# Kernel tuning notes

Measured on AMD Instinct MI355X. Metric: run time of the kernel, lower is better.

Reference implementation:

```python
import jax, jax.numpy as jnp
import numpy as np

B, M, F_IN, DX, K, L, N_ALL = 8192, 10, 128, 128, 64, 32, 100000
NN = M - 1          # n_neigh
INF = float(M)


def layer_norm(x, g, b, eps=1e-5):
    mu = x.mean(-1, keepdims=True)
    var = ((x - mu) ** 2).mean(-1, keepdims=True)
    return (x - mu) * jax.lax.rsqrt(var + eps) * g + b


def bfs_dists(adj, mask):
    # normalized all-pairs hop distances via repeated boolean matmul (m=10 fixed)
    adj_bin = (adj > 1e-5).astype(jnp.float32)
    eye = jnp.eye(M, dtype=bool)
    d = jnp.where(eye[None], 0.0, jnp.where(adj_bin > 0, 1.0, INF))
    curr = adj_bin
    for k in range(2, M):
        curr = jnp.matmul(curr, adj_bin)
        d = jnp.where((curr > 0) & (d == INF), float(k), d)
    mask2 = mask[:, :, None] * mask[:, None, :]
    d = jnp.where(mask2 == 0, INF, d)
    return d / float(M)


def compute_sw(zb, zp, theta, vmask):
    # sliced Wasserstein-2 between batch point clouds [B,NN,d] and prototypes [K,NN,d]
    tn = theta / jnp.linalg.norm(theta, axis=1, keepdims=True)
    pb = jnp.einsum('bmd,ld->bml', zb, tn)
    pp = jnp.einsum('kmd,ld->kml', zp, tn)
    idx = jnp.argsort(pb, axis=1)
    pbs = jnp.take_along_axis(pb, idx, axis=1)
    pps = jnp.sort(pp, axis=1)
    w = jnp.take_along_axis(jnp.broadcast_to(vmask[:, :, None], pb.shape), idx, axis=1)
    w = w / (w.sum(axis=1, keepdims=True) + 1e-9)
    # sum_m w*(pb-pp)^2 expanded to avoid materializing [B,K,NN,L]
    t1 = (w * pbs ** 2).sum(axis=1)                   # [B,L]
    t2 = jnp.einsum('bml,kml->bkl', w * pbs, pps)     # [B,K,L]
    t3 = jnp.einsum('bml,kml->bkl', w, pps ** 2)
    return (t1[:, None, :] - 2.0 * t2 + t3).mean(axis=-1)


def compute_radial(rb, rp, vmask):
    idx = jnp.argsort(rb, axis=1)
    rbs = jnp.take_along_axis(rb, idx, axis=1)
    rps = jnp.sort(rp, axis=1)
    w = jnp.take_along_axis(vmask, idx, axis=1)
    w = w / (w.sum(axis=1, keepdims=True) + 1e-9)
    return (((rbs[:, None, :] - rps[None]) ** 2) * w[:, None, :]).sum(-1)


def setup_inputs() -> dict:
    key = jax.random.key(0)
    ks = jax.random.split(key, 16)
    up = (jax.random.uniform(ks[0], (B, M, M)) < 0.3).astype(jnp.float32)
    adj = jnp.maximum(up, up.transpose(0, 2, 1)) * (1.0 - jnp.eye(M))
    features = jax.random.normal(ks[1], (N_ALL, F_IN), jnp.float32)
    idxs = jax.random.randint(ks[2], (B, M), 0, N_ALL + 1)   # N_ALL == padding index
    rn = lambda k, s, sc=0.02: sc * jax.random.normal(k, s, jnp.float32)
    params = dict(
        x_lin_w=rn(ks[3], (F_IN, DX), 0.05), x_lin_b=jnp.zeros((DX,)),
        x_ln_g=jnp.ones((DX,)), x_ln_b=jnp.zeros((DX,)),
        s_ln_g=jnp.ones((NN,)), s_ln_b=jnp.zeros((NN,)),
        theta_x=jax.random.normal(ks[4], (L, DX), jnp.float32),
        theta_s=jax.random.normal(ks[5], (L, NN), jnp.float32),
        alpha_raw=jnp.zeros(()),
        an_w1=rn(ks[6], (DX, 32), 0.1), an_b1=jnp.zeros((32,)),
        an_w2=rn(ks[7], (32, 1), 0.1), an_b2=jnp.zeros((1,)),
        wn_w1=rn(ks[8], (2 * DX, 32), 0.1), wn_b1=jnp.zeros((32,)),
        wn_w2=rn(ks[9], (32, 1), 0.1), wn_b2=jnp.zeros((1,)),
        w_raw=jnp.zeros(()),
        proto_root=jax.random.normal(ks[10], (K, F_IN), jnp.float32),
        proto_neigh=jax.random.normal(ks[11], (K, NN, F_IN), jnp.float32),
        proto_rad=jax.random.uniform(ks[12], (K, NN)),
        proto_dn=jax.random.uniform(ks[13], (NN * (NN - 1) // 2, K), minval=-0.5, maxval=0.5),
        log_gamma=jnp.asarray(np.log(0.01), jnp.float32),
    )
    return {"adj": adj, "features": features, "idxs": idxs, **params}


def reference(adj, features, idxs, x_lin_w, x_lin_b, x_ln_g, x_ln_b, s_ln_g, s_ln_b,
              theta_x, theta_s, alpha_raw, an_w1, an_b1, an_w2, an_b2,
              wn_w1, wn_b1, wn_w2, wn_b2, w_raw,
              proto_root, proto_neigh, proto_rad, proto_dn, log_gamma):
    b = adj.shape[0]
    x_all = jnp.concatenate([features, jnp.zeros((1, F_IN), features.dtype)], 0)
    x_patch = x_all[idxs]                             # [B,M,F]
    x_root, x_neigh = x_patch[:, 0], x_patch[:, 1:]
    vmask = (idxs[:, 1:] != N_ALL).astype(jnp.float32)   # [B,NN]
    lin = lambda x: x @ x_lin_w + x_lin_b
    h_root = layer_norm(lin(x_root), x_ln_g, x_ln_b)
    h_proto_root = layer_norm(lin(proto_root), x_ln_g, x_ln_b)
    d_root_feat = (jnp.sum(h_root ** 2, -1)[:, None] + jnp.sum(h_proto_root ** 2, -1)[None]
                   - 2.0 * h_root @ h_proto_root.T)   # squared cdist [B,K]
    full_mask = jnp.concatenate([jnp.ones((b, 1), jnp.float32), vmask], 1)
    dists_full = bfs_dists(adj, full_mask)
    d_radial_str = compute_radial(dists_full[:, 0, 1:], proto_rad, vmask)
    h_neigh = layer_norm(lin(x_neigh), x_ln_g, x_ln_b)     # dropout = identity (eval)
    h_proto_neigh = layer_norm(lin(proto_neigh), x_ln_g, x_ln_b)
    sw_neigh_feat = compute_sw(h_neigh, h_proto_neigh, theta_x, vmask)
    hs_neigh = layer_norm(jnp.sort(dists_full[:, 1:, 1:], axis=1), s_ln_g, s_ln_b)
    ti, tj = np.triu_indices(NN, 1)
    C = jnp.zeros((K, NN, NN)).at[:, ti, tj].set(jax.nn.sigmoid(proto_dn).T)
    C = C + C.transpose(0, 2, 1)
    hs_proto = layer_norm(jnp.sort(C, axis=1), s_ln_g, s_ln_b)
    sw_neigh_str = compute_sw(hs_neigh, hs_proto, theta_s, vmask)
    h_pooled = (h_neigh * vmask[:, :, None]).sum(1) / (vmask.sum(1, keepdims=True) + 1e-9)
    alpha_logit = jnp.maximum(h_pooled @ an_w1 + an_b1, 0.0) @ an_w2 + an_b2   # [B,1]
    alpha = jax.nn.sigmoid(alpha_raw + alpha_logit)
    # pairwise w_net([h_root; h_proto_root]) without materializing [B,K,2*DX]
    hb = h_root @ wn_w1[:DX] + wn_b1                   # [B,32]
    hp = h_proto_root @ wn_w1[DX:]                     # [K,32]
    w_logit = (jnp.maximum(hb[:, None] + hp[None], 0.0) @ wn_w2)[..., 0] + wn_b2[0]
    w = jax.nn.sigmoid(w_raw + w_logit)                # [B,K]
    d_feat = w * d_root_feat + (1.0 - w) * sw_neigh_feat
    d_str = w * d_radial_str + (1.0 - w) * sw_neigh_str
    d_fgw = alpha * d_feat + (1.0 - alpha) * d_str
    return jnp.exp(-jnp.exp(log_gamma) * d_fgw)        # [B,K]
```

## Files before the change

### kernel.cpp

```cpp
#include <hip/hip_runtime.h>
#include <hip/hip_bf16.h>

typedef unsigned short u16;
typedef __attribute__((ext_vector_type(8))) short short8;
typedef __attribute__((ext_vector_type(4))) float f32x4;

#define NN 9
#define DX 128
#define KP 64
#define LL 32
#define NALL 100000
#define BMAX 8192
#define NBM 16
#define NBP 64

#define MFMA(a, b, c) __builtin_amdgcn_mfma_f32_16x16x32_bf16(a, b, c, 0, 0, 0)
#define WFENCE() __threadfence_block()

__device__ __align__(16) float g_tns[LL * NN];
__device__ __align__(16) float g_hprn[KP];
__device__ __align__(16) float g_hpt[32 * KP];
__device__ __align__(16) float g_rpst[NN * KP];
__device__ __align__(16) u16   g_hx[BMAX * 10 * DX];
__device__ __align__(16) u16   g_pW[16384];
__device__ __align__(16) u16   g_pBt[4096];
__device__ __align__(16) u16   g_pBr[8192];
__device__ __align__(16) u16   g_pBx[36864];
__device__ __align__(16) u16   g_pBs[36864];
__device__ __align__(16) u16   g_pAn[4096];
__device__ __align__(16) u16   g_pWn[4096];

__device__ __forceinline__ float bf2f(u16 u) {
    union { unsigned u; float f; } v; v.u = ((unsigned)u) << 16; return v.f;
}
__device__ __forceinline__ u16 f2bf(float f) {
    __hip_bfloat16 h = __float2bfloat16(f);
    union { __hip_bfloat16 h; u16 u; } v; v.h = h; return v.u;
}
__device__ __forceinline__ float ldv(const void* p, long i, int f32) {
    return f32 ? ((const float*)p)[i] : bf2f(((const u16*)p)[i]);
}
__device__ __forceinline__ float sigmoidf(float x) { return 1.f / (1.f + expf(-x)); }

__device__ __forceinline__ int bfrag_idx(int ksteps, int ncol, int kd) {
    int ntile = ncol >> 4, n = ncol & 15;
    int kstep = kd >> 5, quad = (kd >> 3) & 3, j = kd & 7;
    return ((ntile * ksteps + kstep) * 64 + quad * 16 + n) * 8 + j;
}

__device__ __forceinline__ void rank9(const float* v, int* r) {
#pragma unroll
    for (int m = 0; m < 9; m++) {
        int rk = 0;
#pragma unroll
        for (int n = 0; n < 9; n++)
            rk += (v[n] < v[m]) || (v[n] == v[m] && n < m);
        r[m] = rk;
    }
}

__global__ __launch_bounds__(256) void k_pack(
    const void* xlw, const void* theta_x, const void* theta_s,
    const void* an_w1, const void* wn_w1, const void* xlg) {
    int t = threadIdx.x;
    const int f32 = (((const u16*)xlg)[0] == 0);
    if (blockIdx.x == 0) {
        for (int i = t; i < 16384; i += 256) {
            int c = i >> 7, d = i & 127;
            g_pW[bfrag_idx(4, d, c)] = f2bf(ldv(xlw, i, f32));
        }
    } else if (blockIdx.x == 1) {
        if (t < 32) {
            float s = 0;
            for (int d = 0; d < 128; d++) { float v = ldv(theta_x, t * 128 + d, f32); s = fmaf(v, v, s); }
            float inv = 1.f / sqrtf(s);
            for (int d = 0; d < 128; d++)
                g_pBt[bfrag_idx(4, t, d)] = f2bf(ldv(theta_x, t * 128 + d, f32) * inv);
        } else if (t < 64) {
            int l = t - 32;
            float s = 0;
            for (int j = 0; j < 9; j++) { float v = ldv(theta_s, l * 9 + j, f32); s = fmaf(v, v, s); }
            float inv = 1.f / sqrtf(s);
            for (int j = 0; j < 9; j++) g_tns[l * 9 + j] = ldv(theta_s, l * 9 + j, f32) * inv;
        }
    } else {
        for (int i = t; i < 4096; i += 256) {
            int d = i >> 5, j = i & 31;
            g_pAn[bfrag_idx(4, j, d)] = f2bf(ldv(an_w1, i, f32));
            g_pWn[bfrag_idx(4, j, d)] = f2bf(ldv(wn_w1, i, f32));
        }
    }
}

__global__ __launch_bounds__(256, 8) void k_lin(
    const void* feat, const int* idxs,
    const void* proto_root, const void* proto_neigh,
    const void* xlb, const void* xlg, const void* xlbt,
    const void* slg, const void* slb, const void* wn_w1,
    const void* proto_rad, const void* proto_dn, int B) {
    __shared__ __align__(16) unsigned char sm[4368];
    u16*   hXpb = (u16*)sm;
    float* pbX  = (float*)(sm + 2560);
    float* Cm   = (float*)(sm + 3712);
    float* hsnP = (float*)(sm + 4040);

    int t = threadIdx.x, lane = t & 63, w = t >> 6;
    const int f32 = (((const u16*)xlg)[0] == 0);
    int fm = lane & 15, quad = lane >> 4;
    bool isProto = (blockIdx.x < (unsigned)NBP);
    int rcap = isProto ? 10 : 60;
    int base = isProto ? blockIdx.x * 10 : (blockIdx.x - NBP) * 60;
    int rowT = isProto ? KP * 10 : B * 10;

    int lr = w * 16 + fm, gr = base + lr;
    bool azero = true;
    const void* abuf = feat; long aoff = 0;
    if (lr < rcap && gr < rowT) {
        if (!isProto) {
            int id = idxs[gr];
            if (id != NALL) { azero = false; aoff = (long)id * 128; }
        } else {
            int rr = gr % 10; azero = false;
            if (rr < 9) { abuf = proto_neigh; aoff = (long)((gr / 10) * 9 + rr) * 128; }
            else        { abuf = proto_root;  aoff = (long)(gr / 10) * 128; }
        }
    }

    if (w * 16 < rcap) {
        f32x4 acc[8];
#pragma unroll
        for (int nt = 0; nt < 8; nt++) acc[nt] = (f32x4){0.f, 0.f, 0.f, 0.f};
#pragma unroll
        for (int ks = 0; ks < 4; ks++) {
            short8 af = {0, 0, 0, 0, 0, 0, 0, 0};
            if (!azero) {
                if (f32) {
                    const f32x4* src = (const f32x4*)((const float*)abuf + aoff + ks * 32 + quad * 8);
                    f32x4 v0 = src[0], v1 = src[1];
                    u16* ap = (u16*)&af;
#pragma unroll
                    for (int j = 0; j < 4; j++) { ap[j] = f2bf(v0[j]); ap[4 + j] = f2bf(v1[j]); }
                } else {
                    af = *(const short8*)((const u16*)abuf + aoff + ks * 32 + quad * 8);
                }
            }
#pragma unroll
            for (int nt = 0; nt < 8; nt++) {
                short8 bf = *(const short8*)(g_pW + ((nt * 4 + ks) * 64 + lane) * 8);
                acc[nt] = MFMA(af, bf, acc[nt]);
            }
        }
        float bias8[8];
#pragma unroll
        for (int nt = 0; nt < 8; nt++) bias8[nt] = ldv(xlb, nt * 16 + fm, f32);
#pragma unroll
        for (int reg = 0; reg < 4; reg++) {
            float s = 0, q = 0;
#pragma unroll
            for (int nt = 0; nt < 8; nt++) {
                float v = acc[nt][reg] + bias8[nt];
                s += v; q = fmaf(v, v, q);
            }
#pragma unroll
            for (int m = 1; m < 16; m <<= 1) { s += __shfl_xor(s, m); q += __shfl_xor(q, m); }
            float mu = s * (1.f / 128.f);
            float var = fmaxf(q * (1.f / 128.f) - mu * mu, 0.f);
            float rs = rsqrtf(var + 1e-5f);
            int rowD = w * 16 + quad * 4 + reg, grD = base + rowD;
            if (rowD < rcap && grD < rowT) {
#pragma unroll
                for (int nt = 0; nt < 8; nt++) {
                    float val = (acc[nt][reg] + bias8[nt] - mu) * rs * ldv(xlg, nt * 16 + fm, f32)
                              + ldv(xlbt, nt * 16 + fm, f32);
                    if (!isProto) g_hx[grD * 128 + nt * 16 + fm] = f2bf(val);
                    else          hXpb[rowD * 128 + nt * 16 + fm] = f2bf(val);
                }
            }
        }
    }
    if (!isProto) return;

    __syncthreads();
    int kb = blockIdx.x;

    for (int i = t; i < 128; i += 256)
        g_pBr[bfrag_idx(4, kb, i)] = hXpb[1152 + i];
    if (w == 0) {
        float v0 = bf2f(hXpb[1152 + lane]);
        float v1 = bf2f(hXpb[1216 + lane]);
        float q = v0 * v0 + v1 * v1;
#pragma unroll
        for (int m = 32; m >= 1; m >>= 1) q += __shfl_xor(q, m);
        if (lane == 0) g_hprn[kb] = q;
    }
    for (int i = t; i < 32; i += 256) {
        float a = 0;
        for (int d = 0; d < 128; d++)
            a = fmaf(bf2f(hXpb[1152 + d]), ldv(wn_w1, (128 + d) * 32 + i, f32), a);
        g_hpt[i * 64 + kb] = a;
    }
    if (t == 0) {
        float v[9]; int r[9];
#pragma unroll
        for (int m = 0; m < 9; m++) v[m] = ldv(proto_rad, kb * 9 + m, f32);
        rank9(v, r);
#pragma unroll
        for (int m = 0; m < 9; m++) g_rpst[r[m] * 64 + kb] = v[m];
    }
    if (w == 0) {
        f32x4 acc0 = {0.f, 0.f, 0.f, 0.f}, acc1 = {0.f, 0.f, 0.f, 0.f};
        const u16* arow = hXpb + fm * 128;
#pragma unroll
        for (int ks = 0; ks < 4; ks++) {
            short8 af = {0, 0, 0, 0, 0, 0, 0, 0};
            if (fm < 9) af = *(const short8*)(arow + ks * 32 + quad * 8);
            short8 b0 = *(const short8*)(g_pBt + ((0 * 4 + ks) * 64 + lane) * 8);
            short8 b1 = *(const short8*)(g_pBt + ((1 * 4 + ks) * 64 + lane) * 8);
            acc0 = MFMA(af, b0, acc0);
            acc1 = MFMA(af, b1, acc1);
        }
#pragma unroll
        for (int reg = 0; reg < 4; reg++) {
            int row = quad * 4 + reg;
            if (row < 9) {
                pbX[row * 32 + fm]      = acc0[reg];
                pbX[row * 32 + 16 + fm] = acc1[reg];
            }
        }
    }
    for (int i = t; i < 81; i += 256) {
        int ii = i / 9, jj = i % 9; float v = 0.f;
        if (ii != jj) {
            int a = (ii < jj) ? ii : jj, b2 = (ii < jj) ? jj : ii;
            int p = a * 8 - a * (a - 1) / 2 + (b2 - a - 1);
            v = sigmoidf(ldv(proto_dn, p * 64 + kb, f32));
        }
        Cm[i] = v;
    }
    __syncthreads();
    if (t < 32) {
        float v[9]; int r[9];
#pragma unroll
        for (int m = 0; m < 9; m++) v[m] = pbX[m * 32 + t];
        rank9(v, r);
#pragma unroll
        for (int m = 0; m < 9; m++) {
            int kd = t * 9 + r[m];
            g_pBx[bfrag_idx(18, kb, kd)]       = f2bf(v[m] * v[m]);
            g_pBx[bfrag_idx(18, kb, 288 + kd)] = f2bf(v[m]);
        }
    }
    if (t >= 64 && t < 73) {
        int col = t - 64;
        float v[9]; int r[9];
#pragma unroll
        for (int j = 0; j < 9; j++) v[j] = Cm[j * 9 + col];
        rank9(v, r);
#pragma unroll
        for (int j = 0; j < 9; j++) Cm[r[j] * 9 + col] = v[j];
    }
    __syncthreads();
    if (t < 9) {
        float mu = 0;
#pragma unroll
        for (int j = 0; j < 9; j++) mu += Cm[t * 9 + j];
        mu *= (1.f / 9.f);
        float var = 0;
#pragma unroll
        for (int j = 0; j < 9; j++) { float d0 = Cm[t * 9 + j] - mu; var = fmaf(d0, d0, var); }
        var *= (1.f / 9.f);
        float rs = rsqrtf(var + 1e-5f);
#pragma unroll
        for (int j = 0; j < 9; j++)
            hsnP[t * 9 + j] = (Cm[t * 9 + j] - mu) * rs * ldv(slg, j, f32) + ldv(slb, j, f32);
    }
    __syncthreads();
    if (t < 32) {
#pragma unroll
        for (int m = 0; m < 9; m++) {
            float a = 0;
#pragma unroll
            for (int j = 0; j < 9; j++) a = fmaf(hsnP[m * 9 + j], g_tns[t * 9 + j], a);
            pbX[m * 32 + t] = a;
        }
    }
    __syncthreads();
    if (t < 32) {
        float v[9]; int r[9];
#pragma unroll
        for (int m = 0; m < 9; m++) v[m] = pbX[m * 32 + t];
        rank9(v, r);
#pragma unroll
        for (int m = 0; m < 9; m++) {
            int kd = t * 9 + r[m];
            g_pBs[bfrag_idx(18, kb, kd)]       = f2bf(v[m] * v[m]);
            g_pBs[bfrag_idx(18, kb, 288 + kd)] = f2bf(v[m]);
        }
    }
}

struct M3 {
    u16   Cf[NBM][584];
    u16   Cs[NBM][584];
    u16   hpoolb[NBM][136];
    float pb[NBM][288];
    float df[NBM][100];
    float hst[NBM][81];
    float drad[NBM][65];
    float hbv[NBM][33];
    float rbss[NBM][9], wrad[NBM][9];
    float sc[NBM][9];
};
__global__ __launch_bounds__(1024, 8) void k_main(
    const void* adj, const int* idxs,
    const void* slg, const void* slb,
    const void* an_b1, const void* an_w2, const void* an_b2,
    const void* wn_b1, const void* wn_w2, const void* wn_b2,
    const void* alpha_raw, const void* w_raw, const void* log_gamma,
    const void* xlg, void* out, int B) {
    __shared__ __align__(16) M3 S;
    int t = threadIdx.x, lane = t & 63, w = t >> 6;
    const int f32 = (((const u16*)xlg)[0] == 0);
    int fm = lane & 15, quad = lane >> 4;
    int bw = blockIdx.x * NBM + w;
    bool bv = (bw < B);

    unsigned long long mb = 0; float nv = 1e-9f, inv = 0.f;

    if (bv) {
        bool valid = false;
        if (lane < 10) {
            int id = idxs[bw * 10 + lane];
            valid = (lane == 0) || (id != NALL);
        }
        mb = __ballot(valid);
        nv = (float)__popcll(mb & 0x3FEull) + 1e-9f;
        inv = 1.f / nv;
        unsigned rowbits = 0;
        if (lane < 10) {
            for (int j = 0; j < 10; j++)
                if (ldv(adj, (long)bw * 100 + lane * 10 + j, f32) > 1e-5f) rowbits |= 1u << j;
        }
        int dl[10];
#pragma unroll
        for (int j = 0; j < 10; j++) dl[j] = (j == lane) ? 0 : (((rowbits >> j) & 1) ? 1 : 10);
        unsigned reach = (lane < 10) ? (rowbits | (1u << lane)) : 0u;
        for (int s = 2; s <= 9; s++) {
            unsigned nr = reach;
#pragma unroll
            for (int j = 0; j < 10; j++) {
                unsigned rj = __shfl(rowbits, j);
                if ((reach >> j) & 1) nr |= rj;
            }
            unsigned add = nr & ~reach;
#pragma unroll
            for (int j = 0; j < 10; j++) if ((add >> j) & 1) dl[j] = s;
            reach = nr;
            if (__all(add == 0)) break;
        }
        if (lane < 10) {
            int mi = (int)((mb >> lane) & 1);
#pragma unroll
            for (int j = 0; j < 10; j++) {
                int mj = (int)((mb >> j) & 1);
                S.df[w][lane * 10 + j] = (mi && mj) ? (float)dl[j] * 0.1f : 1.0f;
            }
        }
        {
            float v[9];
#pragma unroll
            for (int m = 0; m < 9; m++) {
                float vm = ((mb >> (1 + m)) & 1) ? (float)dl[1 + m] * 0.1f : 1.0f;
                v[m] = __shfl(vm, 0);
            }
            if (lane < 9) {
                float mine = v[0];
#pragma unroll
                for (int m = 1; m < 9; m++) if (lane == m) mine = v[m];
                int rk = 0;
#pragma unroll
                for (int n = 0; n < 9; n++) rk += (v[n] < mine) || (v[n] == mine && n < lane);
                S.rbss[w][rk] = mine;
                S.wrad[w][rk] = (((mb >> (1 + lane)) & 1) ? 1.f : 0.f) * inv;
            }
        }
        {
            u16 u0 = g_hx[bw * 1280 + lane], u1 = g_hx[bw * 1280 + 64 + lane];
            float v0 = bf2f(u0), v1 = bf2f(u1);
            float q = v0 * v0 + v1 * v1;
#pragma unroll
            for (int m = 32; m >= 1; m >>= 1) q += __shfl_xor(q, m);
            if (lane == 0) S.sc[w][1] = q;
        }
        for (int dd = lane; dd < 128; dd += 64) {
            float a = 0;
#pragma unroll
            for (int m = 0; m < 9; m++) {
                float hv = bf2f(g_hx[bw * 1280 + (1 + m) * 128 + dd]);
                float msk = ((mb >> (1 + m)) & 1) ? 1.f : 0.f;
                a = fmaf(hv, msk, a);
            }
            S.hpoolb[w][dd] = f2bf(a * inv);
        }
        {
            f32x4 acc0 = {0.f, 0.f, 0.f, 0.f}, acc1 = {0.f, 0.f, 0.f, 0.f};
            const u16* arow = g_hx + (bw * 10 + 1 + fm) * 128;
#pragma unroll
            for (int ks = 0; ks < 4; ks++) {
                short8 af = {0, 0, 0, 0, 0, 0, 0, 0};
                if (fm < 9) af = *(const short8*)(arow + ks * 32 + quad * 8);
                short8 b0 = *(const short8*)(g_pBt + ((0 * 4 + ks) * 64 + lane) * 8);
                short8 b1 = *(const short8*)(g_pBt + ((1 * 4 + ks) * 64 + lane) * 8);
                acc0 = MFMA(af, b0, acc0);
                acc1 = MFMA(af, b1, acc1);
            }
#pragma unroll
            for (int reg = 0; reg < 4; reg++) {
                int row = quad * 4 + reg;
                if (row < 9) {
                    S.pb[w][row * 32 + fm]      = acc0[reg];
                    S.pb[w][row * 32 + 16 + fm] = acc1[reg];
                }
            }
        }
        WFENCE();

        {
            float t1 = 0;
            if (lane < 32) {
                float v[9]; int r[9];
#pragma unroll
                for (int m = 0; m < 9; m++) v[m] = S.pb[w][m * 32 + lane];
                rank9(v, r);
#pragma unroll
                for (int m = 0; m < 9; m++) {
                    float wgt = (((mb >> (1 + m)) & 1) ? 1.f : 0.f) * inv;
                    int slot = lane * 9 + r[m];
                    S.Cf[w][slot]       = f2bf(wgt);
                    S.Cf[w][288 + slot] = f2bf(-2.f * wgt * v[m]);
                    t1 = fmaf(wgt * v[m], v[m], t1);
                }
            }
#pragma unroll
            for (int m = 16; m >= 1; m >>= 1) t1 += __shfl_xor(t1, m);
            if (lane == 0) S.sc[w][3] = t1;
        }
        if (lane < 9) {
            float v[9]; int r[9];
#pragma unroll
            for (int i = 0; i < 9; i++) v[i] = S.df[w][(1 + i) * 10 + 1 + lane];
            rank9(v, r);
#pragma unroll
            for (int i = 0; i < 9; i++) S.hst[w][r[i] * 9 + lane] = v[i];
        }
        {
            float acc = 0;
#pragma unroll
            for (int m = 0; m < 9; m++) {
                float d0 = S.rbss[w][m] - g_rpst[m * 64 + lane];
                acc = fmaf(d0 * d0, S.wrad[w][m], acc);
            }
            S.drad[w][lane] = acc;
        }
        WFENCE();

        if (lane < 9) {
            float vv[9];
#pragma unroll
            for (int j = 0; j < 9; j++) vv[j] = S.hst[w][lane * 9 + j];
            float mu = 0;
#pragma unroll
            for (int j = 0; j < 9; j++) mu += vv[j];
            mu *= (1.f / 9.f);
            float var = 0;
#pragma unroll
            for (int j = 0; j < 9; j++) { float d0 = vv[j] - mu; var = fmaf(d0, d0, var); }
            var *= (1.f / 9.f);
            float rs = rsqrtf(var + 1e-5f);
#pragma unroll
            for (int j = 0; j < 9; j++)
                S.hst[w][lane * 9 + j] = (vv[j] - mu) * rs * ldv(slg, j, f32) + ldv(slb, j, f32);
        }
        WFENCE();

        {
            int l = lane & 31;
            int m0 = (lane < 32) ? 0 : 5, m1 = (lane < 32) ? 5 : 9;
            for (int m = m0; m < m1; m++) {
                float a = 0;
#pragma unroll
                for (int j = 0; j < 9; j++) a = fmaf(S.hst[w][m * 9 + j], g_tns[l * 9 + j], a);
                S.pb[w][m * 32 + l] = a;
            }
        }
        WFENCE();

        {
            float t1 = 0;
            if (lane < 32) {
                float v[9]; int r[9];
#pragma unroll
                for (int m = 0; m < 9; m++) v[m] = S.pb[w][m * 32 + lane];
                rank9(v, r);
#pragma unroll
                for (int m = 0; m < 9; m++) {
                    float wgt = (((mb >> (1 + m)) & 1) ? 1.f : 0.f) * inv;
                    int slot = lane * 9 + r[m];
                    S.Cs[w][slot]       = f2bf(wgt);
                    S.Cs[w][288 + slot] = f2bf(-2.f * wgt * v[m]);
                    t1 = fmaf(wgt * v[m], v[m], t1);
                }
            }
#pragma unroll
            for (int m = 16; m >= 1; m >>= 1) t1 += __shfl_xor(t1, m);
            if (lane == 0) S.sc[w][4] = t1;
        }
    }
    __syncthreads();

    f32x4 rd = {0.f, 0.f, 0.f, 0.f};
    f32x4 accF = {0.f, 0.f, 0.f, 0.f}, accS = {0.f, 0.f, 0.f, 0.f};
    if (w < 4) {
#pragma unroll
        for (int ks = 0; ks < 4; ks++) {
            short8 af = {0, 0, 0, 0, 0, 0, 0, 0};
            int bb = blockIdx.x * NBM + fm;
            if (bb < B) af = *(const short8*)(g_hx + (long)bb * 1280 + ks * 32 + quad * 8);
            short8 bfr = *(const short8*)(g_pBr + ((w * 4 + ks) * 64 + lane) * 8);
            rd = MFMA(af, bfr, rd);
        }
#pragma unroll
        for (int ks = 0; ks < 18; ks++) {
            short8 aF = *(const short8*)(S.Cf[fm] + ks * 32 + quad * 8);
            short8 aS = *(const short8*)(S.Cs[fm] + ks * 32 + quad * 8);
            short8 bF = *(const short8*)(g_pBx + ((w * 18 + ks) * 64 + lane) * 8);
            short8 bS = *(const short8*)(g_pBs + ((w * 18 + ks) * 64 + lane) * 8);
            accF = MFMA(aF, bF, accF);
            accS = MFMA(aS, bS, accS);
        }
    } else if (w == 4) {
        f32x4 a0 = {0.f, 0.f, 0.f, 0.f}, a1 = {0.f, 0.f, 0.f, 0.f};
#pragma unroll
        for (int ks = 0; ks < 4; ks++) {
            short8 af = {0, 0, 0, 0, 0, 0, 0, 0};
            int bb = blockIdx.x * NBM + fm;
            if (bb < B) af = *(const short8*)(g_hx + (long)bb * 1280 + ks * 32 + quad * 8);
            short8 b0 = *(const short8*)(g_pWn + ((0 * 4 + ks) * 64 + lane) * 8);
            short8 b1 = *(const short8*)(g_pWn + ((1 * 4 + ks) * 64 + lane) * 8);
            a0 = MFMA(af, b0, a0);
            a1 = MFMA(af, b1, a1);
        }
        float wb0 = ldv(wn_b1, fm, f32), wb1 = ldv(wn_b1, 16 + fm, f32);
#pragma unroll
        for (int reg = 0; reg < 4; reg++) {
            int b = quad * 4 + reg;
            S.hbv[b][fm]      = a0[reg] + wb0;
            S.hbv[b][16 + fm] = a1[reg] + wb1;
        }
    } else if (w == 5) {
        f32x4 a0 = {0.f, 0.f, 0.f, 0.f}, a1 = {0.f, 0.f, 0.f, 0.f};
#pragma unroll
        for (int ks = 0; ks < 4; ks++) {
            short8 af = *(const short8*)(S.hpoolb[fm] + ks * 32 + quad * 8);
            short8 b0 = *(const short8*)(g_pAn + ((0 * 4 + ks) * 64 + lane) * 8);
            short8 b1 = *(const short8*)(g_pAn + ((1 * 4 + ks) * 64 + lane) * 8);
            a0 = MFMA(af, b0, a0);
            a1 = MFMA(af, b1, a1);
        }
        float ab0 = ldv(an_b1, fm, f32), ab1 = ldv(an_b1, 16 + fm, f32);
        float aw0 = ldv(an_w2, fm, f32), aw1 = ldv(an_w2, 16 + fm, f32);
        float araw = ldv(alpha_raw, 0, f32), ab2 = ldv(an_b2, 0, f32);
#pragma unroll
        for (int reg = 0; reg < 4; reg++) {
            float s = fmaxf(a0[reg] + ab0, 0.f) * aw0 + fmaxf(a1[reg] + ab1, 0.f) * aw1;
            s += __shfl_xor(s, 1); s += __shfl_xor(s, 2);
            s += __shfl_xor(s, 4); s += __shfl_xor(s, 8);
            if (fm == 0) S.sc[quad * 4 + reg][2] = sigmoidf(araw + s + ab2);
        }
    }
    __syncthreads();

    if (w < 4) {
        int k = w * 16 + fm;
        float wb2 = ldv(wn_b2, 0, f32);
        float wr  = ldv(w_raw, 0, f32);
        float gamma = expf(ldv(log_gamma, 0, f32));
        float hprnk = g_hprn[k];
        float wl[4] = {0.f, 0.f, 0.f, 0.f};
#pragma unroll 4
        for (int j = 0; j < 32; j++) {
            float hptv = g_hpt[j * 64 + k];
            float w2v = ldv(wn_w2, j, f32);
#pragma unroll
            for (int reg = 0; reg < 4; reg++)
                wl[reg] = fmaf(fmaxf(S.hbv[quad * 4 + reg][j] + hptv, 0.f), w2v, wl[reg]);
        }
#pragma unroll
        for (int reg = 0; reg < 4; reg++) {
            int b = quad * 4 + reg, bb = blockIdx.x * NBM + b;
            if (bb >= B) continue;
            float swf = (S.sc[b][3] + accF[reg]) * (1.f / 32.f);
            float sws = (S.sc[b][4] + accS[reg]) * (1.f / 32.f);
            float drfk = S.sc[b][1] + hprnk - 2.f * rd[reg];
            float wgt = sigmoidf(wr + wl[reg] + wb2);
            float dfeat = wgt * drfk + (1.f - wgt) * swf;
            float dstr  = wgt * S.drad[b][k] + (1.f - wgt) * sws;
            float al = S.sc[b][2];
            float dfgw = al * dfeat + (1.f - al) * dstr;
            if (!(dfgw == dfgw)) dfgw = 1e30f;
            float res = expf(-gamma * dfgw);
            if (f32) ((float*)out)[(long)bb * 64 + k] = res;
            else     ((u16*)out)[(long)bb * 64 + k] = f2bf(res);
        }
    }
}

extern "C" void kernel_launch(void* const* d_in, const int* in_sizes, int n_in,
                              void* d_out, int out_size, void* d_ws, size_t ws_size,
                              hipStream_t stream) {
    const void* adj  = d_in[0];
    const void* feat = d_in[1];
    const int*  idxs = (const int*)d_in[2];
    const void* xlw  = d_in[3];
    const void* xlb  = d_in[4];
    const void* xlg  = d_in[5];
    const void* xlbt = d_in[6];
    const void* slg  = d_in[7];
    const void* slb  = d_in[8];
    const void* thx  = d_in[9];
    const void* ths  = d_in[10];
    const void* araw = d_in[11];
    const void* anw1 = d_in[12];
    const void* anb1 = d_in[13];
    const void* anw2 = d_in[14];
    const void* anb2 = d_in[15];
    const void* wnw1 = d_in[16];
    const void* wnb1 = d_in[17];
    const void* wnw2 = d_in[18];
    const void* wnb2 = d_in[19];
    const void* wraw = d_in[20];
    const void* prt  = d_in[21];
    const void* prn  = d_in[22];
    const void* prad = d_in[23];
    const void* pdn  = d_in[24];
    const void* lgam = d_in[25];
    int B = in_sizes[2] / 10;
    int NBQ = (B * 10 + 59) / 60;

    k_pack<<<3, 256, 0, stream>>>(xlw, thx, ths, anw1, wnw1, xlg);
    k_lin<<<NBP + NBQ, 256, 0, stream>>>(feat, idxs, prt, prn,
                                         xlb, xlg, xlbt, slg, slb, wnw1,
                                         prad, pdn, B);
    k_main<<<(B + NBM - 1) / NBM, 1024, 0, stream>>>(adj, idxs, slg, slb,
                                  anb1, anw2, anb2, wnb1, wnw2, wnb2,
                                  araw, wraw, lgam, xlg, d_out, B);
}
```

Measured before the change: 227.3 us.

## Stage linear-layer weights in LDS, prefetch A fragments, parallelize proto wn dot

Each block copies the 32KB bf16 weight fragment buffer from global memory into shared memory once, then runs MFMA B-operand reads from LDS. A-fragment loads and the layer-norm gamma/beta/bias loads are hoisted ahead of the barrier so their latency overlaps the weight copy. The per-prototype wn_w1 projection, previously 32 serial threads each doing 128 FMAs, now spreads across all 256 threads with a shuffle reduction. Launch bounds drop occupancy to 4 blocks per CU because of the extra 32KB of LDS, and every block, including the small proto blocks, pays for the copy.

```diff
diff --git a/kernel.cpp b/kernel.cpp
--- a/kernel.cpp
+++ b/kernel.cpp
@@ -92,17 +92,17 @@
     }
 }
 
-__global__ __launch_bounds__(256, 8) void k_lin(
+__global__ __launch_bounds__(256, 4) void k_lin(
     const void* feat, const int* idxs,
     const void* proto_root, const void* proto_neigh,
     const void* xlb, const void* xlg, const void* xlbt,
     const void* slg, const void* slb, const void* wn_w1,
     const void* proto_rad, const void* proto_dn, int B) {
-    __shared__ __align__(16) unsigned char sm[4368];
-    u16*   hXpb = (u16*)sm;
-    float* pbX  = (float*)(sm + 2560);
-    float* Cm   = (float*)(sm + 3712);
-    float* hsnP = (float*)(sm + 4040);
+    __shared__ __align__(16) u16   WfL[16384];
+    __shared__ __align__(16) u16   hXpb[1280];
+    __shared__ __align__(16) float pbX[288];
+    __shared__ __align__(16) float Cm[84];
+    __shared__ __align__(16) float hsnP[84];
 
     int t = threadIdx.x, lane = t & 63, w = t >> 6;
     const int f32 = (((const u16*)xlg)[0] == 0);
@@ -111,6 +111,13 @@
     int rcap = isProto ? 10 : 60;
     int base = isProto ? blockIdx.x * 10 : (blockIdx.x - NBP) * 60;
     int rowT = isProto ? KP * 10 : B * 10;
+
+    {
+        const short8* src = (const short8*)g_pW;
+        short8* dst = (short8*)WfL;
+#pragma unroll
+        for (int i = 0; i < 8; i++) dst[t + 256 * i] = src[t + 256 * i];
+    }
 
     int lr = w * 16 + fm, gr = base + lr;
     bool azero = true;
@@ -125,6 +132,34 @@
             else        { abuf = proto_root;  aoff = (long)(gr / 10) * 128; }
         }
     }
+    short8 af[4];
+#pragma unroll
+    for (int ks = 0; ks < 4; ks++) af[ks] = (short8){0, 0, 0, 0, 0, 0, 0, 0};
+    if (!azero) {
+        if (f32) {
+#pragma unroll
+            for (int ks = 0; ks < 4; ks++) {
+                const f32x4* src = (const f32x4*)((const float*)abuf + aoff + ks * 32 + quad * 8);
+                f32x4 v0 = src[0], v1 = src[1];
+                u16* ap = (u16*)&af[ks];
+#pragma unroll
+                for (int j = 0; j < 4; j++) { ap[j] = f2bf(v0[j]); ap[4 + j] = f2bf(v1[j]); }
+            }
+        } else {
+#pragma unroll
+            for (int ks = 0; ks < 4; ks++)
+                af[ks] = *(const short8*)((const u16*)abuf + aoff + ks * 32 + quad * 8);
+        }
+    }
+    float bias8[8], gg8[8], bb8[8];
+#pragma unroll
+    for (int nt = 0; nt < 8; nt++) {
+        int col = nt * 16 + fm;
+        bias8[nt] = ldv(xlb, col, f32);
+        gg8[nt]   = ldv(xlg, col, f32);
+        bb8[nt]   = ldv(xlbt, col, f32);
+    }
+    __syncthreads();
 
     if (w * 16 < rcap) {
         f32x4 acc[8];
@@ -132,27 +167,12 @@
         for (int nt = 0; nt < 8; nt++) acc[nt] = (f32x4){0.f, 0.f, 0.f, 0.f};
 #pragma unroll
         for (int ks = 0; ks < 4; ks++) {
-            short8 af = {0, 0, 0, 0, 0, 0, 0, 0};
-            if (!azero) {
-                if (f32) {
-                    const f32x4* src = (const f32x4*)((const float*)abuf + aoff + ks * 32 + quad * 8);
-                    f32x4 v0 = src[0], v1 = src[1];
-                    u16* ap = (u16*)&af;
-#pragma unroll
-                    for (int j = 0; j < 4; j++) { ap[j] = f2bf(v0[j]); ap[4 + j] = f2bf(v1[j]); }
-                } else {
-                    af = *(const short8*)((const u16*)abuf + aoff + ks * 32 + quad * 8);
-                }
-            }
 #pragma unroll
             for (int nt = 0; nt < 8; nt++) {
-                short8 bf = *(const short8*)(g_pW + ((nt * 4 + ks) * 64 + lane) * 8);
-                acc[nt] = MFMA(af, bf, acc[nt]);
-            }
-        }
-        float bias8[8];
-#pragma unroll
-        for (int nt = 0; nt < 8; nt++) bias8[nt] = ldv(xlb, nt * 16 + fm, f32);
+                short8 bf = *(const short8*)(WfL + ((nt * 4 + ks) * 64 + lane) * 8);
+                acc[nt] = MFMA(af[ks], bf, acc[nt]);
+            }
+        }
 #pragma unroll
         for (int reg = 0; reg < 4; reg++) {
             float s = 0, q = 0;
@@ -170,8 +190,7 @@
             if (rowD < rcap && grD < rowT) {
 #pragma unroll
                 for (int nt = 0; nt < 8; nt++) {
-                    float val = (acc[nt][reg] + bias8[nt] - mu) * rs * ldv(xlg, nt * 16 + fm, f32)
-                              + ldv(xlbt, nt * 16 + fm, f32);
+                    float val = (acc[nt][reg] + bias8[nt] - mu) * rs * gg8[nt] + bb8[nt];
                     if (!isProto) g_hx[grD * 128 + nt * 16 + fm] = f2bf(val);
                     else          hXpb[rowD * 128 + nt * 16 + fm] = f2bf(val);
                 }
@@ -193,11 +212,18 @@
         for (int m = 32; m >= 1; m >>= 1) q += __shfl_xor(q, m);
         if (lane == 0) g_hprn[kb] = q;
     }
-    for (int i = t; i < 32; i += 256) {
+    {
+        int j = t >> 3, sub = t & 7;
         float a = 0;
-        for (int d = 0; d < 128; d++)
-            a = fmaf(bf2f(hXpb[1152 + d]), ldv(wn_w1, (128 + d) * 32 + i, f32), a);
-        g_hpt[i * 64 + kb] = a;
+#pragma unroll
+        for (int dd = 0; dd < 16; dd++) {
+            int d = sub * 16 + dd;
+            a = fmaf(bf2f(hXpb[1152 + d]), ldv(wn_w1, (128 + d) * 32 + j, f32), a);
+        }
+        a += __shfl_xor(a, 1);
+        a += __shfl_xor(a, 2);
+        a += __shfl_xor(a, 4);
+        if (sub == 0) g_hpt[j * 64 + kb] = a;
     }
     if (t == 0) {
         float v[9]; int r[9];
@@ -212,12 +238,12 @@
         const u16* arow = hXpb + fm * 128;
 #pragma unroll
         for (int ks = 0; ks < 4; ks++) {
-            short8 af = {0, 0, 0, 0, 0, 0, 0, 0};
-            if (fm < 9) af = *(const short8*)(arow + ks * 32 + quad * 8);
+            short8 afp = {0, 0, 0, 0, 0, 0, 0, 0};
+            if (fm < 9) afp = *(const short8*)(arow + ks * 32 + quad * 8);
             short8 b0 = *(const short8*)(g_pBt + ((0 * 4 + ks) * 64 + lane) * 8);
             short8 b1 = *(const short8*)(g_pBt + ((1 * 4 + ks) * 64 + lane) * 8);
-            acc0 = MFMA(af, b0, acc0);
-            acc1 = MFMA(af, b1, acc1);
+            acc0 = MFMA(afp, b0, acc0);
+            acc1 = MFMA(afp, b1, acc1);
         }
 #pragma unroll
         for (int reg = 0; reg < 4; reg++) {
```

Result: faster. 208.9 us, median of 2 (-8.1%).
